# Kernel optimization log

Hardware: AMD Instinct MI355X
Metric: run time of the kernel (lower is better)

The kernel has to match this reference:

```python
import jax, jax.numpy as jnp
import numpy as np

DIM = 1024
NUM_HEADS = 16
HEAD_DIM = DIM // NUM_HEADS
SCALE = HEAD_DIM ** -0.5


def setup_inputs() -> dict:
    key = jax.random.key(0)
    ks = jax.random.split(key, 11)
    B, T = 2, 2048
    std = DIM ** -0.5
    return {
        "query": jax.random.normal(ks[0], (B, T, DIM), jnp.float32),
        "key": jax.random.normal(ks[1], (B, T, DIM), jnp.float32),
        "value": jax.random.normal(ks[2], (B, T, DIM), jnp.float32),
        "wq": jax.random.normal(ks[3], (DIM, DIM), jnp.float32) * std,
        "bq": jnp.zeros((DIM,), jnp.float32),
        "wk": jax.random.normal(ks[4], (DIM, DIM), jnp.float32) * std,
        "bk": jnp.zeros((DIM,), jnp.float32),
        "wv": jax.random.normal(ks[5], (DIM, DIM), jnp.float32) * std,
        "bv": jnp.zeros((DIM,), jnp.float32),
        "wo": jax.random.normal(ks[6], (DIM, DIM), jnp.float32) * std,
        "bo": jnp.zeros((DIM,), jnp.float32),
    }


def reference(query, key, value, wq, bq, wk, bk, wv, bv, wo, bo):
    B, Tq, D = query.shape
    Tk = key.shape[1]
    H, Hd = NUM_HEADS, HEAD_DIM
    # projections (torch Linear: x @ W^T + b); reshape to [B, H, T, Hd]
    q = (query @ wq.T + bq).reshape(B, Tq, H, Hd).transpose(0, 2, 1, 3)
    k = (key @ wk.T + bk).reshape(B, Tk, H, Hd).transpose(0, 2, 1, 3)
    v = (value @ wv.T + bv).reshape(B, Tk, H, Hd).transpose(0, 2, 1, 3)
    # attention scores [B, H, Tq, Tk]
    attn = jnp.einsum("bhqd,bhkd->bhqk", q, k) * SCALE
    attn = jax.nn.softmax(attn, axis=-1)
    # dropout p=0.0 -> identity
    out = jnp.einsum("bhqk,bhkd->bhqd", attn, v)
    out = out.transpose(0, 2, 1, 3).reshape(B, Tq, D)
    return out @ wo.T + bo
```

## Files before the change

### kernel.cpp

```cpp
#include <hip/hip_runtime.h>
#include <math.h>


typedef __attribute__((ext_vector_type(8))) short short8;
typedef __attribute__((ext_vector_type(4))) float f32x4;
typedef __attribute__((ext_vector_type(4))) float float4v;
typedef __attribute__((ext_vector_type(4))) unsigned short ushort4v;
typedef __attribute__((ext_vector_type(2))) unsigned int uint2v;

typedef __attribute__((address_space(3))) unsigned int lds_uint;
typedef __attribute__((address_space(1))) unsigned int glb_uint;

__device__ __forceinline__ void gload_lds16(const void* g, void* l) {
    __builtin_amdgcn_global_load_lds((glb_uint*)(unsigned long long)g,
                                     (lds_uint*)(unsigned int)(unsigned long long)l,
                                     16, 0, 0);
}

__device__ __forceinline__ unsigned short f32_bf16(float f) {
    union { float f; unsigned int u; } x; x.f = f;
    unsigned int r = x.u + 0x7fffu + ((x.u >> 16) & 1u);
    return (unsigned short)(r >> 16);
}

__device__ __forceinline__ unsigned int cvt_pk_bf16(float lo, float hi) {
    unsigned int r;
    asm("v_cvt_pk_bf16_f32 %0, %1, %2" : "=v"(r) : "v"(lo), "v"(hi));
    return r;
}

__device__ __forceinline__ float exp2_fast(float x) {
    float r;
    asm("v_exp_f32 %0, %1" : "=v"(r) : "v"(x));
    return r;
}

#define QSCALE 0.18033688011112042f

__global__ void pack3_bf16(const float* __restrict__ a, const float* __restrict__ b,
                           const float* __restrict__ c,
                           unsigned short* __restrict__ oa, unsigned short* __restrict__ ob,
                           unsigned short* __restrict__ oc, int n4) {
    const int y = blockIdx.y;
    const float* in = (y == 0) ? a : (y == 1) ? b : c;
    unsigned short* out = (y == 0) ? oa : (y == 1) ? ob : oc;
    int i = blockIdx.x * blockDim.x + threadIdx.x;
    if (i < n4) {
        float4v v = ((const float4v*)in)[i];
        ushort4v o;
        o.x = f32_bf16(v.x); o.y = f32_bf16(v.y);
        o.z = f32_bf16(v.z); o.w = f32_bf16(v.w);
        ((ushort4v*)out)[i] = o;
    }
}

__global__ void pack4_bf16(const float* __restrict__ a, const float* __restrict__ b,
                           const float* __restrict__ c, const float* __restrict__ d,
                           unsigned short* __restrict__ oa, unsigned short* __restrict__ ob,
                           unsigned short* __restrict__ oc, unsigned short* __restrict__ od,
                           int n4) {
    const int y = blockIdx.y;
    const float* in = (y == 0) ? a : (y == 1) ? b : (y == 2) ? c : d;
    unsigned short* out = (y == 0) ? oa : (y == 1) ? ob : (y == 2) ? oc : od;
    int i = blockIdx.x * blockDim.x + threadIdx.x;
    if (i < n4) {
        float4v v = ((const float4v*)in)[i];
        ushort4v o;
        o.x = f32_bf16(v.x); o.y = f32_bf16(v.y);
        o.z = f32_bf16(v.z); o.w = f32_bf16(v.w);
        ((ushort4v*)out)[i] = o;
    }
}

__global__ __launch_bounds__(256, 2) void gemm_qkv(
    const unsigned short* __restrict__ A0, const unsigned short* __restrict__ A1,
    const unsigned short* __restrict__ A2,
    const unsigned short* __restrict__ W0, const unsigned short* __restrict__ W1,
    const unsigned short* __restrict__ W2,
    const float* __restrict__ bs0, const float* __restrict__ bs1,
    const float* __restrict__ bs2,
    unsigned short* __restrict__ O0, unsigned short* __restrict__ O1,
    unsigned short* __restrict__ O2)
{
    const int z = blockIdx.z;
    const unsigned short* A = (z == 0) ? A0 : (z == 1) ? A1 : A2;
    const unsigned short* W = (z == 0) ? W0 : (z == 1) ? W1 : W2;
    const float* bias        = (z == 0) ? bs0 : (z == 1) ? bs1 : bs2;
    unsigned short* C        = (z == 0) ? O0 : (z == 1) ? O1 : O2;
    const float oscale = (z == 0) ? QSCALE : 1.0f;
    const int N = 1024, K = 1024;

    __shared__ unsigned short As[128 * 64];
    __shared__ unsigned short Bs[128 * 64];
    const int tid  = threadIdx.x;
    const int lane = tid & 63, wave = tid >> 6;
    const int l15 = lane & 15, l4 = lane >> 4;
    const int bm = blockIdx.y * 128, bn = blockIdx.x * 128;
    const int wr = wave >> 1, wc = wave & 1;

    f32x4 acc[4][4];
    #pragma unroll
    for (int i = 0; i < 4; ++i)
        #pragma unroll
        for (int j = 0; j < 4; ++j)
            #pragma unroll
            for (int e = 0; e < 4; ++e) acc[i][j][e] = 0.f;

    const int srow = lane >> 3;
    const int scol = (lane & 7) * 8;

    for (int k0 = 0; k0 < K; k0 += 64) {
        __syncthreads();
        #pragma unroll
        for (int i = 0; i < 4; ++i) {
            int c = wave * 4 + i;
            int row = c * 8 + srow;
            gload_lds16(A + (size_t)(bm + row) * K + k0 + scol, &As[c * 512]);
            gload_lds16(W + (size_t)(bn + row) * K + k0 + scol, &Bs[c * 512]);
        }
        __syncthreads();
        #pragma unroll
        for (int kk = 0; kk < 2; ++kk) {
            short8 af[4], bf[4];
            const int ko = kk * 32 + l4 * 8;
            #pragma unroll
            for (int i = 0; i < 4; ++i)
                af[i] = *(const short8*)&As[(wr * 64 + i * 16 + l15) * 64 + ko];
            #pragma unroll
            for (int j = 0; j < 4; ++j)
                bf[j] = *(const short8*)&Bs[(wc * 64 + j * 16 + l15) * 64 + ko];
            #pragma unroll
            for (int i = 0; i < 4; ++i)
                #pragma unroll
                for (int j = 0; j < 4; ++j)
                    acc[i][j] = __builtin_amdgcn_mfma_f32_16x16x32_bf16(
                        af[i], bf[j], acc[i][j], 0, 0, 0);
        }
    }

    #pragma unroll
    for (int j = 0; j < 4; ++j) {
        const int col = bn + wc * 64 + j * 16 + l15;
        const float bj = bias[col];
        #pragma unroll
        for (int i = 0; i < 4; ++i) {
            const int row0 = bm + wr * 64 + i * 16 + l4 * 4;
            #pragma unroll
            for (int r = 0; r < 4; ++r) {
                const int row = row0 + r;
                const float v = (acc[i][j][r] + bj) * oscale;
                if (z < 2) {
                    C[(size_t)row * N + col] = f32_bf16(v);
                } else {
                    const int b = row >> 11, t = row & 2047;
                    C[(((size_t)((b << 4) + (col >> 6)) * 64
                        + (col & 63)) << 11) + t] = f32_bf16(v);
                }
            }
        }
    }
}

__global__ __launch_bounds__(256, 3) void gemm_out(
    const unsigned short* __restrict__ A,
    const unsigned short* __restrict__ W,
    const float* __restrict__ bias,
    float* __restrict__ C)
{
    const int N = 1024, K = 1024;
    __shared__ unsigned short As[2][64 * 64];
    __shared__ unsigned short Bs[2][128 * 64];
    const int tid  = threadIdx.x;
    const int lane = tid & 63, wave = tid >> 6;
    const int l15 = lane & 15, l4 = lane >> 4;
    const int bm = blockIdx.y * 64, bn = blockIdx.x * 128;
    const int wr = wave >> 1, wc = wave & 1;

    f32x4 acc[2][4];
    #pragma unroll
    for (int i = 0; i < 2; ++i)
        #pragma unroll
        for (int j = 0; j < 4; ++j)
            #pragma unroll
            for (int e = 0; e < 4; ++e) acc[i][j][e] = 0.f;

    const int srow = lane >> 3;
    const int scol = (lane & 7) * 8;

    auto stage = [&](int bf, int k0) {
        #pragma unroll
        for (int i = 0; i < 2; ++i) {
            const int c = wave * 2 + i;
            gload_lds16(A + (size_t)(bm + c * 8 + srow) * K + k0 + scol,
                        &As[bf][c * 512]);
        }
        #pragma unroll
        for (int i = 0; i < 4; ++i) {
            const int c = wave * 4 + i;
            gload_lds16(W + (size_t)(bn + c * 8 + srow) * K + k0 + scol,
                        &Bs[bf][c * 512]);
        }
    };

    stage(0, 0);
    __syncthreads();

    int bufi = 0;
    for (int k0 = 0; k0 < K; k0 += 64) {
        if (k0 + 64 < K) stage(bufi ^ 1, k0 + 64);
        #pragma unroll
        for (int kk = 0; kk < 2; ++kk) {
            short8 af[2], bf[4];
            const int ko = kk * 32 + l4 * 8;
            #pragma unroll
            for (int i = 0; i < 2; ++i)
                af[i] = *(const short8*)&As[bufi][(wr * 32 + i * 16 + l15) * 64 + ko];
            #pragma unroll
            for (int j = 0; j < 4; ++j)
                bf[j] = *(const short8*)&Bs[bufi][(wc * 64 + j * 16 + l15) * 64 + ko];
            #pragma unroll
            for (int i = 0; i < 2; ++i)
                #pragma unroll
                for (int j = 0; j < 4; ++j)
                    acc[i][j] = __builtin_amdgcn_mfma_f32_16x16x32_bf16(
                        af[i], bf[j], acc[i][j], 0, 0, 0);
        }
        __syncthreads();
        bufi ^= 1;
    }

    #pragma unroll
    for (int j = 0; j < 4; ++j) {
        const int col = bn + wc * 64 + j * 16 + l15;
        const float bj = bias[col];
        #pragma unroll
        for (int i = 0; i < 2; ++i) {
            const int row0 = bm + wr * 32 + i * 16 + l4 * 4;
            #pragma unroll
            for (int r = 0; r < 4; ++r)
                C[(size_t)(row0 + r) * N + col] = acc[i][j][r] + bj;
        }
    }
}

__global__ __launch_bounds__(256, 4) void attn_fwd(
    const unsigned short* __restrict__ qp,
    const unsigned short* __restrict__ kp,
    const unsigned short* __restrict__ vt,
    unsigned short* __restrict__ op)
{
    __shared__ unsigned short Ks[2][64 * 64];
    __shared__ unsigned short Vs[2][64 * 64];
    __shared__ unsigned short P[4][16 * 64];

    const int tid = threadIdx.x;
    const int lane = tid & 63, wave = tid >> 6;
    const int l15 = lane & 15, l4 = lane >> 4;
    const int swz = (l15 & 7) << 3;

    const int flat = blockIdx.y * 32 + blockIdx.x;
    const int swzb = (flat & 7) * 128 + (flat >> 3);
    const int bx = swzb & 31;
    const int bh = swzb >> 5;
    const int b = bh >> 4, h = bh & 15;
    const int q0 = bx * 64 + wave * 16;

    const size_t xbase = (size_t)b * 2048 * 1024 + h * 64;
    const size_t vbase = (size_t)bh * 64 * 2048;

    const int sr = lane >> 3;
    const int sc = ((lane & 7) ^ sr) * 8;

    short8 bq[2];
    #pragma unroll
    for (int kk = 0; kk < 2; ++kk)
        bq[kk] = *(const short8*)&qp[xbase
            + (size_t)(q0 + l15) * 1024 + kk * 32 + l4 * 8];

    f32x4 acc[4];
    #pragma unroll
    for (int dj = 0; dj < 4; ++dj)
        #pragma unroll
        for (int e = 0; e < 4; ++e) acc[dj][e] = 0.f;

    float m_run = -1e30f, l_run = 0.f;

    {
        const int c0 = wave * 2;
        #pragma unroll
        for (int i = 0; i < 2; ++i) {
            const int c = c0 + i;
            gload_lds16(kp + xbase + (size_t)(c * 8 + sr) * 1024 + sc,
                        &Ks[0][c * 512]);
            gload_lds16(vt + vbase + (size_t)(c * 8 + sr) * 2048 + sc,
                        &Vs[0][c * 512]);
        }
    }
    __syncthreads();

    const int NT = 2048 / 64;
    int buf = 0;
    for (int t = 0; t < NT; ++t) {
        const int kv0 = t * 64;
        if (t + 1 < NT) {
            const int c0 = wave * 2;
            #pragma unroll
            for (int i = 0; i < 2; ++i) {
                const int c = c0 + i;
                gload_lds16(kp + xbase + (size_t)(kv0 + 64 + c * 8 + sr) * 1024 + sc,
                            &Ks[buf ^ 1][c * 512]);
                gload_lds16(vt + vbase + (size_t)(c * 8 + sr) * 2048 + kv0 + 64 + sc,
                            &Vs[buf ^ 1][c * 512]);
            }
        }

        f32x4 st[4];
        {
            short8 ak[4];
            #pragma unroll
            for (int j = 0; j < 4; ++j)
                ak[j] = *(const short8*)&Ks[buf][(j * 16 + l15) * 64
                                                 + ((l4 << 3) ^ swz)];
            const f32x4 z4 = {0.f, 0.f, 0.f, 0.f};
            __builtin_amdgcn_s_setprio(1);
            #pragma unroll
            for (int j = 0; j < 4; ++j)
                st[j] = __builtin_amdgcn_mfma_f32_16x16x32_bf16(
                    ak[j], bq[0], z4, 0, 0, 0);
            __builtin_amdgcn_s_setprio(0);
            #pragma unroll
            for (int j = 0; j < 4; ++j)
                ak[j] = *(const short8*)&Ks[buf][(j * 16 + l15) * 64
                                                 + (((4 + l4) << 3) ^ swz)];
            __builtin_amdgcn_s_setprio(1);
            #pragma unroll
            for (int j = 0; j < 4; ++j)
                st[j] = __builtin_amdgcn_mfma_f32_16x16x32_bf16(
                    ak[j], bq[1], st[j], 0, 0, 0);
            __builtin_amdgcn_s_setprio(0);
        }

        short8 av[2][4];
        #pragma unroll
        for (int kvc = 0; kvc < 2; ++kvc)
            #pragma unroll
            for (int dj = 0; dj < 4; ++dj)
                av[kvc][dj] = *(const short8*)&Vs[buf][(dj * 16 + l15) * 64
                                                 + (((kvc * 4 + l4) << 3) ^ swz)];

        {
            float tm[4];
            #pragma unroll
            for (int j = 0; j < 4; ++j)
                tm[j] = fmaxf(fmaxf(st[j][0], st[j][1]),
                              fmaxf(st[j][2], st[j][3]));
            float mx = fmaxf(fmaxf(tm[0], tm[1]), fmaxf(tm[2], tm[3]));
            mx = fmaxf(mx, __shfl_xor(mx, 16));
            mx = fmaxf(mx, __shfl_xor(mx, 32));
            const float mnew = fmaxf(m_run, mx);
            const float corr = exp2_fast(m_run - mnew);
            m_run = mnew;
            float ts[4];
            #pragma unroll
            for (int j = 0; j < 4; ++j) {
                float p0 = exp2_fast(st[j][0] - mnew);
                float p1 = exp2_fast(st[j][1] - mnew);
                float p2 = exp2_fast(st[j][2] - mnew);
                float p3 = exp2_fast(st[j][3] - mnew);
                st[j][0] = p0; st[j][1] = p1; st[j][2] = p2; st[j][3] = p3;
                ts[j] = (p0 + p1) + (p2 + p3);
            }
            float ls = (ts[0] + ts[1]) + (ts[2] + ts[3]);
            ls += __shfl_xor(ls, 16);
            ls += __shfl_xor(ls, 32);
            l_run = l_run * corr + ls;
            #pragma unroll
            for (int dj = 0; dj < 4; ++dj) acc[dj] *= corr;
        }

        #pragma unroll
        for (int j = 0; j < 4; ++j) {
            uint2v w;
            w.x = cvt_pk_bf16(st[j][0], st[j][1]);
            w.y = cvt_pk_bf16(st[j][2], st[j][3]);
            *(uint2v*)&P[wave][l15 * 64 + ((j * 16 + l4 * 4) ^ swz)] = w;
        }

        #pragma unroll
        for (int kvc = 0; kvc < 2; ++kvc) {
            short8 pb = *(const short8*)&P[wave][l15 * 64
                                                + (((kvc * 4 + l4) << 3) ^ swz)];
            __builtin_amdgcn_s_setprio(1);
            #pragma unroll
            for (int dj = 0; dj < 4; ++dj)
                acc[dj] = __builtin_amdgcn_mfma_f32_16x16x32_bf16(
                    av[kvc][dj], pb, acc[dj], 0, 0, 0);
            __builtin_amdgcn_s_setprio(0);
        }

        __syncthreads();
        buf ^= 1;
    }

    {
        const float inv = 1.0f / l_run;
        const int t = q0 + l15;
        #pragma unroll
        for (int dj = 0; dj < 4; ++dj) {
            uint2v w;
            w.x = cvt_pk_bf16(acc[dj][0] * inv, acc[dj][1] * inv);
            w.y = cvt_pk_bf16(acc[dj][2] * inv, acc[dj][3] * inv);
            *(uint2v*)&op[((size_t)(b * 2048 + t)) * 1024
                          + h * 64 + dj * 16 + l4 * 4] = w;
        }
    }
}

extern "C" void kernel_launch(void* const* d_in, const int* in_sizes, int n_in,
                              void* d_out, int out_size, void* d_ws, size_t ws_size,
                              hipStream_t stream)
{
    const float* q  = (const float*)d_in[0];
    const float* k  = (const float*)d_in[1];
    const float* v  = (const float*)d_in[2];
    const float* wq = (const float*)d_in[3];
    const float* bq = (const float*)d_in[4];
    const float* wk = (const float*)d_in[5];
    const float* bk = (const float*)d_in[6];
    const float* wv = (const float*)d_in[7];
    const float* bv = (const float*)d_in[8];
    const float* wo = (const float*)d_in[9];
    const float* bo = (const float*)d_in[10];
    float* out = (float*)d_out;

    const int M = 4096, N = 1024, K = 1024;
    unsigned char* ws = (unsigned char*)d_ws;
    const size_t SX = (size_t)M * K * 2;
    const size_t SW = (size_t)N * K * 2;
    unsigned short* xq  = (unsigned short*)(ws);
    unsigned short* xk  = (unsigned short*)(ws + SX);
    unsigned short* xv  = (unsigned short*)(ws + 2 * SX);
    unsigned short* wqb = (unsigned short*)(ws + 3 * SX);
    unsigned short* wkb = (unsigned short*)(ws + 3 * SX + SW);
    unsigned short* wvb = (unsigned short*)(ws + 3 * SX + 2 * SW);
    unsigned short* wob = (unsigned short*)(ws + 3 * SX + 3 * SW);
    unsigned short* qp  = (unsigned short*)(ws + 3 * SX + 4 * SW);
    unsigned short* kp  = qp + (size_t)M * N;
    unsigned short* vt  = kp + (size_t)M * N;
    unsigned short* opb = vt + (size_t)M * N;

    pack3_bf16<<<dim3(4096, 3), 256, 0, stream>>>(q, k, v, xq, xk, xv,
                                                  M * K / 4);
    pack4_bf16<<<dim3(1024, 4), 256, 0, stream>>>(wq, wk, wv, wo,
                                                  wqb, wkb, wvb, wob, N * K / 4);

    gemm_qkv<<<dim3(8, 32, 3), 256, 0, stream>>>(xq, xk, xv, wqb, wkb, wvb,
                                                 bq, bk, bv, qp, kp, vt);

    attn_fwd<<<dim3(32, 32), 256, 0, stream>>>(qp, kp, vt, opb);

    gemm_out<<<dim3(8, 64), 256, 0, stream>>>(opb, wob, bo, out);
}
```

Before: 144.1 us.

## Fuse fp32-to-bf16 activation conversion into QKV GEMM and drop setprio in attention

The separate pack kernel that converted query/key/value activations to bf16 is removed. The QKV GEMM now streams fp32 activations straight into LDS and converts them to bf16 in registers before the MFMA. This saves one kernel launch and the write and re-read of three bf16 activation copies. In exchange it doubles the LDS footprint and global traffic for the A tile inside the GEMM and adds conversion ALU work; the s_setprio hints around the MFMAs in attention are also removed.

```diff
diff --git a/kernel.cpp b/kernel.cpp
--- a/kernel.cpp
+++ b/kernel.cpp
@@ -36,23 +36,6 @@
 }
 
 #define QSCALE 0.18033688011112042f
-
-__global__ void pack3_bf16(const float* __restrict__ a, const float* __restrict__ b,
-                           const float* __restrict__ c,
-                           unsigned short* __restrict__ oa, unsigned short* __restrict__ ob,
-                           unsigned short* __restrict__ oc, int n4) {
-    const int y = blockIdx.y;
-    const float* in = (y == 0) ? a : (y == 1) ? b : c;
-    unsigned short* out = (y == 0) ? oa : (y == 1) ? ob : oc;
-    int i = blockIdx.x * blockDim.x + threadIdx.x;
-    if (i < n4) {
-        float4v v = ((const float4v*)in)[i];
-        ushort4v o;
-        o.x = f32_bf16(v.x); o.y = f32_bf16(v.y);
-        o.z = f32_bf16(v.z); o.w = f32_bf16(v.w);
-        ((ushort4v*)out)[i] = o;
-    }
-}
 
 __global__ void pack4_bf16(const float* __restrict__ a, const float* __restrict__ b,
                            const float* __restrict__ c, const float* __restrict__ d,
@@ -73,8 +56,8 @@
 }
 
 __global__ __launch_bounds__(256, 2) void gemm_qkv(
-    const unsigned short* __restrict__ A0, const unsigned short* __restrict__ A1,
-    const unsigned short* __restrict__ A2,
+    const float* __restrict__ A0, const float* __restrict__ A1,
+    const float* __restrict__ A2,
     const unsigned short* __restrict__ W0, const unsigned short* __restrict__ W1,
     const unsigned short* __restrict__ W2,
     const float* __restrict__ bs0, const float* __restrict__ bs1,
@@ -83,14 +66,14 @@
     unsigned short* __restrict__ O2)
 {
     const int z = blockIdx.z;
-    const unsigned short* A = (z == 0) ? A0 : (z == 1) ? A1 : A2;
-    const unsigned short* W = (z == 0) ? W0 : (z == 1) ? W1 : W2;
+    const float* A           = (z == 0) ? A0 : (z == 1) ? A1 : A2;
+    const unsigned short* W  = (z == 0) ? W0 : (z == 1) ? W1 : W2;
     const float* bias        = (z == 0) ? bs0 : (z == 1) ? bs1 : bs2;
     unsigned short* C        = (z == 0) ? O0 : (z == 1) ? O1 : O2;
     const float oscale = (z == 0) ? QSCALE : 1.0f;
     const int N = 1024, K = 1024;
 
-    __shared__ unsigned short As[128 * 64];
+    __shared__ float          Asf[128 * 64];
     __shared__ unsigned short Bs[128 * 64];
     const int tid  = threadIdx.x;
     const int lane = tid & 63, wave = tid >> 6;
@@ -106,17 +89,24 @@
             #pragma unroll
             for (int e = 0; e < 4; ++e) acc[i][j][e] = 0.f;
 
-    const int srow = lane >> 3;
-    const int scol = (lane & 7) * 8;
+    const int srowW = lane >> 3;
+    const int scolW = (lane & 7) * 8;
+    const int arow = lane >> 4;
+    const int acol = (lane & 15) * 4;
 
     for (int k0 = 0; k0 < K; k0 += 64) {
         __syncthreads();
         #pragma unroll
+        for (int i = 0; i < 8; ++i) {
+            const int c = wave * 8 + i;
+            gload_lds16(A + (size_t)(bm + c * 4 + arow) * K + k0 + acol,
+                        &Asf[c * 256]);
+        }
+        #pragma unroll
         for (int i = 0; i < 4; ++i) {
-            int c = wave * 4 + i;
-            int row = c * 8 + srow;
-            gload_lds16(A + (size_t)(bm + row) * K + k0 + scol, &As[c * 512]);
-            gload_lds16(W + (size_t)(bn + row) * K + k0 + scol, &Bs[c * 512]);
+            const int c = wave * 4 + i;
+            gload_lds16(W + (size_t)(bn + c * 8 + srowW) * K + k0 + scolW,
+                        &Bs[c * 512]);
         }
         __syncthreads();
         #pragma unroll
@@ -124,8 +114,18 @@
             short8 af[4], bf[4];
             const int ko = kk * 32 + l4 * 8;
             #pragma unroll
-            for (int i = 0; i < 4; ++i)
-                af[i] = *(const short8*)&As[(wr * 64 + i * 16 + l15) * 64 + ko];
+            for (int i = 0; i < 4; ++i) {
+                const float4v fa0 = *(const float4v*)
+                    &Asf[(wr * 64 + i * 16 + l15) * 64 + ko];
+                const float4v fa1 = *(const float4v*)
+                    &Asf[(wr * 64 + i * 16 + l15) * 64 + ko + 4];
+                union { unsigned int u[4]; short8 s; } cv;
+                cv.u[0] = cvt_pk_bf16(fa0.x, fa0.y);
+                cv.u[1] = cvt_pk_bf16(fa0.z, fa0.w);
+                cv.u[2] = cvt_pk_bf16(fa1.x, fa1.y);
+                cv.u[3] = cvt_pk_bf16(fa1.z, fa1.w);
+                af[i] = cv.s;
+            }
             #pragma unroll
             for (int j = 0; j < 4; ++j)
                 bf[j] = *(const short8*)&Bs[(wc * 64 + j * 16 + l15) * 64 + ko];
@@ -322,22 +322,18 @@
                 ak[j] = *(const short8*)&Ks[buf][(j * 16 + l15) * 64
                                                  + ((l4 << 3) ^ swz)];
             const f32x4 z4 = {0.f, 0.f, 0.f, 0.f};
-            __builtin_amdgcn_s_setprio(1);
             #pragma unroll
             for (int j = 0; j < 4; ++j)
                 st[j] = __builtin_amdgcn_mfma_f32_16x16x32_bf16(
                     ak[j], bq[0], z4, 0, 0, 0);
-            __builtin_amdgcn_s_setprio(0);
             #pragma unroll
             for (int j = 0; j < 4; ++j)
                 ak[j] = *(const short8*)&Ks[buf][(j * 16 + l15) * 64
                                                  + (((4 + l4) << 3) ^ swz)];
-            __builtin_amdgcn_s_setprio(1);
             #pragma unroll
             for (int j = 0; j < 4; ++j)
                 st[j] = __builtin_amdgcn_mfma_f32_16x16x32_bf16(
                     ak[j], bq[1], st[j], 0, 0, 0);
-            __builtin_amdgcn_s_setprio(0);
         }
 
         short8 av[2][4];
@@ -390,12 +386,10 @@
         for (int kvc = 0; kvc < 2; ++kvc) {
             short8 pb = *(const short8*)&P[wave][l15 * 64
                                                 + (((kvc * 4 + l4) << 3) ^ swz)];
-            __builtin_amdgcn_s_setprio(1);
             #pragma unroll
             for (int dj = 0; dj < 4; ++dj)
                 acc[dj] = __builtin_amdgcn_mfma_f32_16x16x32_bf16(
                     av[kvc][dj], pb, acc[dj], 0, 0, 0);
-            __builtin_amdgcn_s_setprio(0);
         }
 
         __syncthreads();
@@ -433,28 +427,23 @@
     const float* bo = (const float*)d_in[10];
     float* out = (float*)d_out;
 
-    const int M = 4096, N = 1024, K = 1024;
+    const int M = 4096, N = 1024;
     unsigned char* ws = (unsigned char*)d_ws;
-    const size_t SX = (size_t)M * K * 2;
-    const size_t SW = (size_t)N * K * 2;
-    unsigned short* xq  = (unsigned short*)(ws);
-    unsigned short* xk  = (unsigned short*)(ws + SX);
-    unsigned short* xv  = (unsigned short*)(ws + 2 * SX);
-    unsigned short* wqb = (unsigned short*)(ws + 3 * SX);
-    unsigned short* wkb = (unsigned short*)(ws + 3 * SX + SW);
-    unsigned short* wvb = (unsigned short*)(ws + 3 * SX + 2 * SW);
-    unsigned short* wob = (unsigned short*)(ws + 3 * SX + 3 * SW);
-    unsigned short* qp  = (unsigned short*)(ws + 3 * SX + 4 * SW);
+    const size_t SW = (size_t)N * 1024 * 2;
+    unsigned short* wqb = (unsigned short*)(ws);
+    unsigned short* wkb = (unsigned short*)(ws + SW);
+    unsigned short* wvb = (unsigned short*)(ws + 2 * SW);
+    unsigned short* wob = (unsigned short*)(ws + 3 * SW);
+    unsigned short* qp  = (unsigned short*)(ws + 4 * SW);
     unsigned short* kp  = qp + (size_t)M * N;
     unsigned short* vt  = kp + (size_t)M * N;
     unsigned short* opb = vt + (size_t)M * N;
 
-    pack3_bf16<<<dim3(4096, 3), 256, 0, stream>>>(q, k, v, xq, xk, xv,
-                                                  M * K / 4);
     pack4_bf16<<<dim3(1024, 4), 256, 0, stream>>>(wq, wk, wv, wo,
-                                                  wqb, wkb, wvb, wob, N * K / 4);
-
-    gemm_qkv<<<dim3(8, 32, 3), 256, 0, stream>>>(xq, xk, xv, wqb, wkb, wvb,
+                                                  wqb, wkb, wvb, wob,
+                                                  N * 1024 / 4);
+
+    gemm_qkv<<<dim3(8, 32, 3), 256, 0, stream>>>(q, k, v, wqb, wkb, wvb,
                                                  bq, bk, bv, qp, kp, vt);
 
     attn_fwd<<<dim3(32, 32), 256, 0, stream>>>(qp, kp, vt, opb);
```

Measured after the change: 159.9 us. 1.11x slower.
